# Optimization experiments

Measured on AMD Instinct MI355X. Metric: run time of the kernel, lower is better.

The kernel has to match this reference:

```python
import jax, jax.numpy as jnp
import numpy as np

B, T, D = 2, 2048, 1024
H, G, K = 16, 4, 64          # num_heads, num_kv_heads, head_dim
R = H // G                   # GQA repeat factor
F = 4096                     # mlp_dim
EPS = 1e-6


def rms_norm(x, scale, eps=EPS):
    var = jnp.mean(x.astype(jnp.float32) ** 2, axis=-1, keepdims=True)
    normed = x * jax.lax.rsqrt(var + eps)
    return (scale * normed).astype(x.dtype)


def apply_rope(x_BTHK, sin_BTK, cos_BTK):
    half = x_BTHK.shape[-1] // 2
    x1, x2 = x_BTHK[..., :half], x_BTHK[..., half:]
    s = sin_BTK[:, :, None, :]
    c = cos_BTK[:, :, None, :]
    return jnp.concatenate([x1 * c - x2 * s, x2 * c + x1 * s], axis=-1).astype(x_BTHK.dtype)


def setup_inputs() -> dict:
    key = jax.random.key(0)
    ks = jax.random.split(key, 12)
    hidden_BTD = jax.random.normal(ks[0], (B, T, D), jnp.float32)
    # rope tables: realistic sin/cos of position*inv_freq
    inv_freq = 1.0 / (10000.0 ** (jnp.arange(K // 2, dtype=jnp.float32) / (K // 2)))
    ang = jnp.arange(T, dtype=jnp.float32)[:, None] * inv_freq[None, :]  # [T, K/2]
    sin_BTK = jnp.broadcast_to(jnp.sin(ang)[None], (B, T, K // 2))
    cos_BTK = jnp.broadcast_to(jnp.cos(ang)[None], (B, T, K // 2))
    mask = jnp.broadcast_to(jnp.tril(jnp.ones((T, T), bool))[None], (B, T, T))
    sc = 1.0 / np.sqrt(D)
    scf = 1.0 / np.sqrt(F)
    return {
        "hidden_BTD": hidden_BTD, "sin_BTK": sin_BTK, "cos_BTK": cos_BTK, "mask": mask,
        "ln1_scale": jnp.ones((D,), jnp.float32),
        "ln2_scale": jnp.ones((D,), jnp.float32),
        "qn_scale": jnp.ones((K,), jnp.float32),
        "kn_scale": jnp.ones((K,), jnp.float32),
        "q_w": jax.random.normal(ks[1], (D, H * K), jnp.float32) * sc,
        "k_w": jax.random.normal(ks[2], (D, G * K), jnp.float32) * sc,
        "v_w": jax.random.normal(ks[3], (D, G * K), jnp.float32) * sc,
        "o_w": jax.random.normal(ks[4], (H * K, D), jnp.float32) * sc,
        "gate_w": jax.random.normal(ks[5], (D, F), jnp.float32) * sc,
        "up_w": jax.random.normal(ks[6], (D, F), jnp.float32) * sc,
        "down_w": jax.random.normal(ks[7], (F, D), jnp.float32) * scf,
    }


def reference(hidden_BTD, sin_BTK, cos_BTK, mask, ln1_scale, ln2_scale,
              qn_scale, kn_scale, q_w, k_w, v_w, o_w, gate_w, up_w, down_w):
    x = rms_norm(hidden_BTD, ln1_scale)
    q = rms_norm((x @ q_w).reshape(B, T, H, K), qn_scale)
    k = rms_norm((x @ k_w).reshape(B, T, G, K), kn_scale)
    v = (x @ v_w).reshape(B, T, G, K)
    q = apply_rope(q, sin_BTK, cos_BTK)
    k = apply_rope(k, sin_BTK, cos_BTK)
    q_BTGRK = q.reshape(B, T, G, R, K)
    scale = K ** (-0.5)
    logits = jnp.einsum('BTGRK,BSGK->BTSGR', q_BTGRK, k) * scale
    neg = float(jnp.finfo(logits.dtype).min)
    logits = jnp.where(mask[:, :, :, None, None], logits, neg)
    weights = jax.nn.softmax(logits.astype(jnp.float32), axis=2).astype(logits.dtype)
    attn = jnp.einsum('BTSGR,BSGK->BTGRK', weights, v).reshape(B, T, H * K)
    hidden_BTD = hidden_BTD + attn @ o_w
    y = rms_norm(hidden_BTD, ln2_scale)
    ff = (jax.nn.silu(y @ gate_w) * (y @ up_w)) @ down_w
    return hidden_BTD + ff
```

## Files before the change

### kernel.cpp

```cpp
#include <hip/hip_runtime.h>
#include <hip/hip_bf16.h>

#define EPSF 1e-6f
constexpr int Bsz  = 2;
constexpr int Tseq = 2048;
constexpr int Dmod = 1024;
constexpr int Hh   = 16;
constexpr int Gg   = 4;
constexpr int Ff   = 4096;
constexpr int Mrows = Bsz * Tseq;

typedef __attribute__((ext_vector_type(8))) short bf16x8;
typedef __attribute__((ext_vector_type(4))) float f32x4;
typedef unsigned short u16;

__device__ inline u16 f2bf(float x) {
    union { float f; unsigned u; } v; v.f = x;
    unsigned r = v.u + 0x7fff + ((v.u >> 16) & 1);
    return (u16)(r >> 16);
}
__device__ inline float bf2f(u16 h) {
    union { unsigned u; float f; } v; v.u = ((unsigned)h) << 16; return v.f;
}

__device__ __forceinline__ void async_copy16(const u16* g, u16* l) {
    __builtin_amdgcn_global_load_lds(
        (const __attribute__((address_space(1))) void*)g,
        (__attribute__((address_space(3))) void*)l, 16, 0, 0);
}


__global__ __launch_bounds__(256) void wprep_all_kernel(
    const float* __restrict__ q_w, const float* __restrict__ k_w,
    const float* __restrict__ v_w, const float* __restrict__ o_w,
    const float* __restrict__ gate_w, const float* __restrict__ up_w,
    const float* __restrict__ down_w,
    const float* __restrict__ hidden, const float* __restrict__ ln1,
    u16* __restrict__ QKVT, u16* __restrict__ OTh, u16* __restrict__ OTl,
    u16* __restrict__ GTh, u16* __restrict__ UTh, u16* __restrict__ DTh,
    u16* __restrict__ Xh)
{
    const int bx = blockIdx.x;

    if (bx >= 14848) {
        const int row = bx - 14848;
        const int tid = threadIdx.x;
        const float4 v = reinterpret_cast<const float4*>(hidden + (size_t)row * Dmod)[tid];
        float ss = v.x * v.x + v.y * v.y + v.z * v.z + v.w * v.w;
        #pragma unroll
        for (int off = 32; off; off >>= 1) ss += __shfl_xor(ss, off, 64);
        __shared__ float part[4];
        if ((tid & 63) == 0) part[tid >> 6] = ss;
        __syncthreads();
        const float tot = part[0] + part[1] + part[2] + part[3];
        const float rstd = rsqrtf(tot * (1.0f / Dmod) + EPSF);
        const float4 sc = reinterpret_cast<const float4*>(ln1)[tid];
        ushort4 h;
        h.x = f2bf(v.x * rstd * sc.x); h.y = f2bf(v.y * rstd * sc.y);
        h.z = f2bf(v.z * rstd * sc.z); h.w = f2bf(v.w * rstd * sc.w);
        *reinterpret_cast<ushort4*>(&Xh[(size_t)row * Dmod + tid * 4]) = h;
        return;
    }

    const float* W; u16* Th; u16* Tl = nullptr;
    int N, Kd, ntile, ktile, drow;
    if (bx < 1024) {
        W = q_w; N = 1024; Kd = 1024; ntile = bx & 31; ktile = bx >> 5;
        Th = QKVT; drow = ntile * 32;
    } else if (bx < 1280) {
        const int i = bx - 1024;
        W = k_w; N = 256; Kd = 1024; ntile = i & 7; ktile = i >> 3;
        Th = QKVT; drow = 1024 + ntile * 32;
    } else if (bx < 1536) {
        const int i = bx - 1280;
        W = v_w; N = 256; Kd = 1024; ntile = i & 7; ktile = i >> 3;
        Th = QKVT; drow = 1280 + ntile * 32;
    } else if (bx < 2560) {
        const int i = bx - 1536;
        W = o_w; N = 1024; Kd = 1024; ntile = i & 31; ktile = i >> 5;
        Th = OTh; Tl = OTl; drow = ntile * 32;
    } else if (bx < 6656) {
        const int i = bx - 2560;
        W = gate_w; N = 4096; Kd = 1024; ntile = i & 127; ktile = i >> 7;
        Th = GTh; drow = ntile * 32;
    } else if (bx < 10752) {
        const int i = bx - 6656;
        W = up_w; N = 4096; Kd = 1024; ntile = i & 127; ktile = i >> 7;
        Th = UTh; drow = ntile * 32;
    } else {
        const int i = bx - 10752;
        W = down_w; N = 1024; Kd = 4096; ntile = i & 31; ktile = i >> 5;
        Th = DTh; drow = ntile * 32;
    }
    const int n0 = ntile * 32, k0 = ktile * 32;

    __shared__ float tile[32][33];
    const int r = threadIdx.x >> 3, c4 = (threadIdx.x & 7) * 4;
    const float4 v = *reinterpret_cast<const float4*>(&W[(size_t)(k0 + r) * N + n0 + c4]);
    tile[r][c4 + 0] = v.x; tile[r][c4 + 1] = v.y;
    tile[r][c4 + 2] = v.z; tile[r][c4 + 3] = v.w;
    __syncthreads();
    const int nl = threadIdx.x >> 3, kq = (threadIdx.x & 7) * 4;
    float x0 = tile[kq + 0][nl], x1 = tile[kq + 1][nl];
    float x2 = tile[kq + 2][nl], x3 = tile[kq + 3][nl];
    ushort4 h;
    h.x = f2bf(x0); h.y = f2bf(x1); h.z = f2bf(x2); h.w = f2bf(x3);
    *reinterpret_cast<ushort4*>(&Th[(size_t)(drow + nl) * Kd + k0 + kq]) = h;
    if (Tl) {
        ushort4 l;
        l.x = f2bf(x0 - bf2f(h.x)); l.y = f2bf(x1 - bf2f(h.y));
        l.z = f2bf(x2 - bf2f(h.z)); l.w = f2bf(x3 - bf2f(h.w));
        *reinterpret_cast<ushort4*>(&Tl[(size_t)(drow + nl) * Kd + k0 + kq]) = l;
    }
}

template <int LO>
__global__ __launch_bounds__(256) void rmsnorm_split_kernel(
    const float* __restrict__ x, const float* __restrict__ scale,
    u16* __restrict__ oh, u16* __restrict__ ol)
{
    const int row = blockIdx.x;
    const int tid = threadIdx.x;
    const float4 v = reinterpret_cast<const float4*>(x + (size_t)row * Dmod)[tid];
    float ss = v.x * v.x + v.y * v.y + v.z * v.z + v.w * v.w;
    #pragma unroll
    for (int off = 32; off; off >>= 1) ss += __shfl_xor(ss, off, 64);
    __shared__ float part[4];
    if ((tid & 63) == 0) part[tid >> 6] = ss;
    __syncthreads();
    const float tot = part[0] + part[1] + part[2] + part[3];
    const float rstd = rsqrtf(tot * (1.0f / Dmod) + EPSF);
    const float4 sc = reinterpret_cast<const float4*>(scale)[tid];
    float o0 = v.x * rstd * sc.x, o1 = v.y * rstd * sc.y;
    float o2 = v.z * rstd * sc.z, o3 = v.w * rstd * sc.w;
    ushort4 h;
    h.x = f2bf(o0); h.y = f2bf(o1); h.z = f2bf(o2); h.w = f2bf(o3);
    *reinterpret_cast<ushort4*>(&oh[(size_t)row * Dmod + tid * 4]) = h;
    if (LO) {
        ushort4 l;
        l.x = f2bf(o0 - bf2f(h.x)); l.y = f2bf(o1 - bf2f(h.y));
        l.z = f2bf(o2 - bf2f(h.z)); l.w = f2bf(o3 - bf2f(h.w));
        *reinterpret_cast<ushort4*>(&ol[(size_t)row * Dmod + tid * 4]) = l;
    }
}

template <int NKT, int BN, int ASPLIT, int BSPLIT, int RES>
__global__ __launch_bounds__(256, 2) void mfma_gemm_pipe(
    const u16* __restrict__ Ah, const u16* __restrict__ Al,
    const u16* __restrict__ Bh, const u16* __restrict__ Bl,
    const float* __restrict__ res, float* __restrict__ C,
    int M, int N)
{
    constexpr int Kd = NKT * 32;
    constexpr int NT = (BN / 2) / 16;
    constexpr int NI = 2 + 2 * ASPLIT + (BN / 64) + (BN / 64) * BSPLIT;
    static_assert(NKT % 4 == 0 && NKT >= 8, "4-buffer rotation");

    __shared__ u16 AsH[4][128 * 32];
    __shared__ u16 BsH[4][BN * 32];
    __shared__ u16 AsL[ASPLIT ? 4 : 1][128 * 32];
    __shared__ u16 BsL[BSPLIT ? 4 : 1][BN * 32];

    const int tid = threadIdx.x;
    const int lane = tid & 63, wave = tid >> 6;
    const int wm = (wave >> 1) * 64, wn = (wave & 1) * (BN / 2);
    const int m0 = blockIdx.y * 128, n0 = blockIdx.x * BN;
    const int fm = lane & 15, quad = lane >> 4;
    const int fsw = (fm >> 1) & 3;
    const int fcol = (quad ^ fsw) * 8;

    f32x4 acc[4][NT];
    #pragma unroll
    for (int i = 0; i < 4; ++i)
        #pragma unroll
        for (int j = 0; j < NT; ++j) acc[i][j] = (f32x4){0.f, 0.f, 0.f, 0.f};

    const int srow = tid >> 2;
    const int schk = tid & 3;
    const int sw   = schk ^ ((srow >> 1) & 3);
    const u16* aS0 = &Ah[(size_t)(m0 + srow) * Kd + sw * 8];
    const u16* aS1 = &Ah[(size_t)(m0 + srow + 64) * Kd + sw * 8];
    const u16* bS0 = &Bh[(size_t)(n0 + srow) * Kd + sw * 8];
    const u16* bS1 = (BN == 128) ? &Bh[(size_t)(n0 + srow + 64) * Kd + sw * 8] : nullptr;
    const u16* alS0 = ASPLIT ? &Al[(size_t)(m0 + srow) * Kd + sw * 8] : nullptr;
    const u16* alS1 = ASPLIT ? &Al[(size_t)(m0 + srow + 64) * Kd + sw * 8] : nullptr;
    const u16* blS0 = BSPLIT ? &Bl[(size_t)(n0 + srow) * Kd + sw * 8] : nullptr;
    const u16* blS1 = (BSPLIT && BN == 128) ? &Bl[(size_t)(n0 + srow + 64) * Kd + sw * 8] : nullptr;
    const int dst0 = srow * 32 + schk * 8;
    const int dst1 = dst0 + 64 * 32;

#define PSTAGE(T, BUF) do {                                                  \
        async_copy16(aS0 + (T) * 32, &AsH[BUF][dst0]);                       \
        async_copy16(aS1 + (T) * 32, &AsH[BUF][dst1]);                       \
        if (ASPLIT) {                                                        \
            async_copy16(alS0 + (T) * 32, &AsL[BUF][dst0]);                  \
            async_copy16(alS1 + (T) * 32, &AsL[BUF][dst1]);                  \
        }                                                                    \
        async_copy16(bS0 + (T) * 32, &BsH[BUF][dst0]);                       \
        if (BN == 128) async_copy16(bS1 + (T) * 32, &BsH[BUF][dst1]);        \
        if (BSPLIT) {                                                        \
            async_copy16(blS0 + (T) * 32, &BsL[BUF][dst0]);                  \
            if (BN == 128) async_copy16(blS1 + (T) * 32, &BsL[BUF][dst1]);   \
        }                                                                    \
    } while (0)

#define PGATE(GATE) do {                                                     \
        if ((GATE) == 2) {                                                   \
            if constexpr (NI == 4)                                           \
                asm volatile("s_waitcnt vmcnt(8)" ::: "memory");             \
            else                                                             \
                asm volatile("s_waitcnt vmcnt(16)" ::: "memory");            \
        } else if ((GATE) == 1) {                                            \
            if constexpr (NI == 4)                                           \
                asm volatile("s_waitcnt vmcnt(4)" ::: "memory");             \
            else                                                             \
                asm volatile("s_waitcnt vmcnt(8)" ::: "memory");             \
        } else if ((GATE) == 0) {                                            \
            asm volatile("s_waitcnt vmcnt(0)" ::: "memory");                 \
        }                                                                    \
    } while (0)

#define PSTEP(BC, BN_, T, PF, GATE) do {                                     \
    bf16x8 ah[4], bh[NT], al[4], bl[NT];                                     \
    _Pragma("unroll")                                                        \
    for (int t = 0; t < 4; ++t) {                                            \
        const int ra = (wm + t * 16 + fm) * 32 + fcol;                       \
        ah[t] = *reinterpret_cast<const bf16x8*>(&AsH[BC][ra]);              \
        if (ASPLIT) al[t] = *reinterpret_cast<const bf16x8*>(&AsL[BC][ra]);  \
    }                                                                        \
    _Pragma("unroll")                                                        \
    for (int t = 0; t < NT; ++t) {                                           \
        const int rb = (wn + t * 16 + fm) * 32 + fcol;                       \
        bh[t] = *reinterpret_cast<const bf16x8*>(&BsH[BC][rb]);              \
        if (BSPLIT) bl[t] = *reinterpret_cast<const bf16x8*>(&BsL[BC][rb]);  \
    }                                                                        \
    if (PF) PSTAGE((T) + 3, BN_);                                            \
    __builtin_amdgcn_s_setprio(1);                                           \
    _Pragma("unroll")                                                        \
    for (int mt = 0; mt < 4; ++mt)                                           \
        _Pragma("unroll")                                                    \
        for (int nt = 0; nt < NT; ++nt) {                                    \
            acc[mt][nt] = __builtin_amdgcn_mfma_f32_16x16x32_bf16(           \
                ah[mt], bh[nt], acc[mt][nt], 0, 0, 0);                       \
            if (BSPLIT)                                                      \
                acc[mt][nt] = __builtin_amdgcn_mfma_f32_16x16x32_bf16(       \
                    ah[mt], bl[nt], acc[mt][nt], 0, 0, 0);                   \
            if (ASPLIT)                                                      \
                acc[mt][nt] = __builtin_amdgcn_mfma_f32_16x16x32_bf16(       \
                    al[mt], bh[nt], acc[mt][nt], 0, 0, 0);                   \
        }                                                                    \
    __builtin_amdgcn_s_setprio(0);                                           \
    PGATE(GATE);                                                             \
    __builtin_amdgcn_s_barrier();                                            \
} while (0)

    PSTAGE(0, 0);
    PSTAGE(1, 1);
    PSTAGE(2, 2);
    PGATE(2);
    __builtin_amdgcn_s_barrier();

    #pragma unroll 1
    for (int t4 = 0; t4 < NKT - 4; t4 += 4) {
        PSTEP((t4 + 0) & 3, (t4 + 3) & 3, t4 + 0, true, 2);
        PSTEP((t4 + 1) & 3, (t4 + 0) & 3, t4 + 1, true, 2);
        PSTEP((t4 + 2) & 3, (t4 + 1) & 3, t4 + 2, true, 2);
        PSTEP((t4 + 3) & 3, (t4 + 2) & 3, t4 + 3, true, 2);
    }
    PSTEP(0, 3, NKT - 4, true, 2);
    PSTEP(1, 0, NKT - 3, false, 1);
    PSTEP(2, 1, NKT - 2, false, 0);
    PSTEP(3, 2, NKT - 1, false, -1);

#undef PSTEP
#undef PGATE
#undef PSTAGE

    const int cr = (lane >> 4) * 4, cn = lane & 15;
    #pragma unroll
    for (int mt = 0; mt < 4; ++mt)
        #pragma unroll
        for (int nt = 0; nt < NT; ++nt)
            #pragma unroll
            for (int r = 0; r < 4; ++r) {
                const int gm = m0 + wm + mt * 16 + cr + r;
                const int gn = n0 + wn + nt * 16 + cn;
                float v = acc[mt][nt][r];
                if (RES) v += res[(size_t)gm * N + gn];
                C[(size_t)gm * N + gn] = v;
            }
}

__global__ __launch_bounds__(256, 2) void qkv_fused_kernel(
    const u16* __restrict__ Ah, const u16* __restrict__ Bh,
    const float* __restrict__ qn, const float* __restrict__ kn,
    const float* __restrict__ sinp, const float* __restrict__ cosp,
    u16* __restrict__ Qbh, u16* __restrict__ Qbl,
    u16* __restrict__ Kbh, u16* __restrict__ Kbl,
    u16* __restrict__ Vth, u16* __restrict__ Vtl)
{
    constexpr int Kd = 1024;
    constexpr int NKT = 32;
    __shared__ u16 As[4][128 * 32];
    __shared__ u16 Bs[4][128 * 32];

    const int tid = threadIdx.x;
    const int lane = tid & 63, wave = tid >> 6;
    const int wm = (wave >> 1) * 64, wn = (wave & 1) * 64;
    const int m0 = blockIdx.y * 128, n0 = blockIdx.x * 128;
    const int fm = lane & 15, quad = lane >> 4;
    const int fsw = (fm >> 1) & 3;
    const int fcol = ((quad ^ fsw) * 8);

    f32x4 acc[4][4];
    #pragma unroll
    for (int i = 0; i < 4; ++i)
        #pragma unroll
        for (int j = 0; j < 4; ++j) acc[i][j] = (f32x4){0.f, 0.f, 0.f, 0.f};

    const int srow = tid >> 2;
    const int schk = tid & 3;
    const int sw   = schk ^ ((srow >> 1) & 3);
    const u16* aS0 = &Ah[(size_t)(m0 + srow) * Kd + sw * 8];
    const u16* aS1 = &Ah[(size_t)(m0 + srow + 64) * Kd + sw * 8];
    const u16* bS0 = &Bh[(size_t)(n0 + srow) * Kd + sw * 8];
    const u16* bS1 = &Bh[(size_t)(n0 + srow + 64) * Kd + sw * 8];
    const int dst0 = srow * 32 + schk * 8;
    const int dst1 = dst0 + 64 * 32;

#define QSTAGE(T, BUF) do {                                                  \
        async_copy16(aS0 + (T) * 32, &As[BUF][dst0]);                        \
        async_copy16(aS1 + (T) * 32, &As[BUF][dst1]);                        \
        async_copy16(bS0 + (T) * 32, &Bs[BUF][dst0]);                        \
        async_copy16(bS1 + (T) * 32, &Bs[BUF][dst1]);                        \
    } while (0)

#define QSTEP(BC, BN, T, PF, GATE) do {                                      \
    bf16x8 ah[4], bh[4];                                                     \
    _Pragma("unroll")                                                        \
    for (int t = 0; t < 4; ++t) {                                            \
        ah[t] = *reinterpret_cast<const bf16x8*>(                            \
            &As[BC][(wm + t * 16 + fm) * 32 + fcol]);                        \
        bh[t] = *reinterpret_cast<const bf16x8*>(                            \
            &Bs[BC][(wn + t * 16 + fm) * 32 + fcol]);                        \
    }                                                                        \
    if (PF) QSTAGE((T) + 3, BN);                                             \
    __builtin_amdgcn_s_setprio(1);                                           \
    _Pragma("unroll")                                                        \
    for (int mt = 0; mt < 4; ++mt)                                           \
        _Pragma("unroll")                                                    \
        for (int nt = 0; nt < 4; ++nt)                                       \
            acc[mt][nt] = __builtin_amdgcn_mfma_f32_16x16x32_bf16(           \
                ah[mt], bh[nt], acc[mt][nt], 0, 0, 0);                       \
    __builtin_amdgcn_s_setprio(0);                                           \
    if ((GATE) == 2) {                                                       \
        asm volatile("s_waitcnt vmcnt(8)" ::: "memory");                     \
    } else if ((GATE) == 1) {                                                \
        asm volatile("s_waitcnt vmcnt(4)" ::: "memory");                     \
    } else if ((GATE) == 0) {                                                \
        asm volatile("s_waitcnt vmcnt(0)" ::: "memory");                     \
    }                                                                        \
    __builtin_amdgcn_s_barrier();                                            \
} while (0)

    QSTAGE(0, 0);
    QSTAGE(1, 1);
    QSTAGE(2, 2);
    asm volatile("s_waitcnt vmcnt(8)" ::: "memory");
    __builtin_amdgcn_s_barrier();

    #pragma unroll 1
    for (int t4 = 0; t4 < NKT - 4; t4 += 4) {
        QSTEP((t4 + 0) & 3, (t4 + 3) & 3, t4 + 0, true, 2);
        QSTEP((t4 + 1) & 3, (t4 + 0) & 3, t4 + 1, true, 2);
        QSTEP((t4 + 2) & 3, (t4 + 1) & 3, t4 + 2, true, 2);
        QSTEP((t4 + 3) & 3, (t4 + 2) & 3, t4 + 3, true, 2);
    }
    QSTEP(0, 3, NKT - 4, true, 2);
    QSTEP(1, 0, NKT - 3, false, 1);
    QSTEP(2, 1, NKT - 2, false, 0);
    QSTEP(3, 2, NKT - 1, false, -1);

#undef QSTEP
#undef QSTAGE

    const int gn0 = n0 + wn;
    const int l15 = lane & 15;

    if (gn0 < 1280) {
        const bool isQ = (gn0 < 1024);
        const float* nsc = isQ ? qn : kn;
        const float osc = isQ ? 0.125f : 1.0f;
        u16* __restrict__ oh = isQ ? Qbh : Kbh;
        u16* __restrict__ ol = isQ ? Qbl : Kbl;
        const int rowstride = isQ ? 1024 : 256;
        const int colbase = isQ ? gn0 : gn0 - 1024;
        float sc[4];
        #pragma unroll
        for (int nt = 0; nt < 4; ++nt) sc[nt] = nsc[nt * 16 + l15];

        #pragma unroll
        for (int mt = 0; mt < 4; ++mt)
            #pragma unroll
            for (int r = 0; r < 4; ++r) {
                const int bt = m0 + wm + mt * 16 + quad * 4 + r;
                float v[4];
                #pragma unroll
                for (int nt = 0; nt < 4; ++nt) v[nt] = acc[mt][nt][r];
                float ss = v[0] * v[0] + v[1] * v[1] + v[2] * v[2] + v[3] * v[3];
                #pragma unroll
                for (int off = 1; off < 16; off <<= 1)
                    ss += __shfl_xor(ss, off, 16);
                const float rstd = rsqrtf(ss * (1.0f / 64.0f) + EPSF);
                float nv[4];
                #pragma unroll
                for (int nt = 0; nt < 4; ++nt) nv[nt] = v[nt] * rstd * sc[nt];
                const float s0 = sinp[bt * 32 + l15];
                const float c0 = cosp[bt * 32 + l15];
                const float s1 = sinp[bt * 32 + 16 + l15];
                const float c1 = cosp[bt * 32 + 16 + l15];
                float o[4];
                o[0] = (nv[0] * c0 - nv[2] * s0) * osc;
                o[1] = (nv[1] * c1 - nv[3] * s1) * osc;
                o[2] = (nv[2] * c0 + nv[0] * s0) * osc;
                o[3] = (nv[3] * c1 + nv[1] * s1) * osc;
                #pragma unroll
                for (int nt = 0; nt < 4; ++nt) {
                    const size_t off = (size_t)bt * rowstride + colbase + nt * 16 + l15;
                    const u16 hi = f2bf(o[nt]);
                    oh[off] = hi;
                    ol[off] = f2bf(o[nt] - bf2f(hi));
                }
            }
    } else {
        const int g = (gn0 - 1280) >> 6;
        const int b = (m0 + wm) >> 11;
        const int tb = ((m0 + wm) & 2047) + quad * 4;
        #pragma unroll
        for (int mt = 0; mt < 4; ++mt)
            #pragma unroll
            for (int nt = 0; nt < 4; ++nt) {
                const float v0 = acc[mt][nt][0], v1 = acc[mt][nt][1];
                const float v2 = acc[mt][nt][2], v3 = acc[mt][nt][3];
                ushort4 hv, lv;
                hv.x = f2bf(v0); hv.y = f2bf(v1); hv.z = f2bf(v2); hv.w = f2bf(v3);
                lv.x = f2bf(v0 - bf2f(hv.x)); lv.y = f2bf(v1 - bf2f(hv.y));
                lv.z = f2bf(v2 - bf2f(hv.z)); lv.w = f2bf(v3 - bf2f(hv.w));
                const size_t off =
                    ((size_t)((b * 4 + g) * 64 + nt * 16 + l15)) * Tseq + tb + mt * 16;
                *reinterpret_cast<ushort4*>(&Vth[off]) = hv;
                *reinterpret_cast<ushort4*>(&Vtl[off]) = lv;
            }
    }
}

#define GU_MFMA4(MBASE, AF)                                                      \
    _Pragma("unroll")                                                            \
    for (int mf = 0; mf < 4; ++mf) {                                             \
        accg[(MBASE) + mf][0] = __builtin_amdgcn_mfma_f32_16x16x32_bf16(         \
            AF[mf], bgf[0], accg[(MBASE) + mf][0], 0, 0, 0);                     \
        accu[(MBASE) + mf][0] = __builtin_amdgcn_mfma_f32_16x16x32_bf16(         \
            AF[mf], buf2[0], accu[(MBASE) + mf][0], 0, 0, 0);                    \
        accg[(MBASE) + mf][1] = __builtin_amdgcn_mfma_f32_16x16x32_bf16(         \
            AF[mf], bgf[1], accg[(MBASE) + mf][1], 0, 0, 0);                     \
        accu[(MBASE) + mf][1] = __builtin_amdgcn_mfma_f32_16x16x32_bf16(         \
            AF[mf], buf2[1], accu[(MBASE) + mf][1], 0, 0, 0);                    \
    }

__global__ __launch_bounds__(512, 2) void gateup8_kernel(
    const u16* __restrict__ Yh, const u16* __restrict__ Yl,
    const u16* __restrict__ Gw, const u16* __restrict__ Uw,
    u16* __restrict__ FF)
{
    constexpr int NK = 32;
    __shared__ u16 AsH[3][256 * 32];
    __shared__ u16 AsL[3][256 * 32];
    __shared__ u16 Gs[3][128 * 32];
    __shared__ u16 Us[3][128 * 32];

    const int tid  = threadIdx.x;
    const int lane = tid & 63;
    const int wave = tid >> 6;
    const int wave_m = wave >> 2;
    const int wave_n = wave & 3;

    const int wg  = blockIdx.x;
    const int xcd = wg & 7;
    const int idx = wg >> 3;
    const int ntile = xcd * 4 + (idx & 3);
    const int mtile = idx >> 2;
    const int m0 = mtile * 256, n0 = ntile * 128;

    const int fm = lane & 15, quad = lane >> 4;
    const int fsw = (fm >> 1) & 3;
    const int fcol = (quad ^ fsw) * 8;

    f32x4 accg[8][2], accu[8][2];
    #pragma unroll
    for (int i = 0; i < 8; ++i)
        #pragma unroll
        for (int j = 0; j < 2; ++j) {
            accg[i][j] = (f32x4){0.f, 0.f, 0.f, 0.f};
            accu[i][j] = (f32x4){0.f, 0.f, 0.f, 0.f};
        }

    const int srow = tid >> 2;
    const int schk = tid & 3;
    const int sw   = schk ^ ((srow >> 1) & 3);
    const u16* aSrc0 = &Yh[(size_t)(m0 + srow) * 1024 + sw * 8];
    const u16* aSrc1 = &Yh[(size_t)(m0 + srow + 128) * 1024 + sw * 8];
    const u16* lSrc0 = &Yl[(size_t)(m0 + srow) * 1024 + sw * 8];
    const u16* lSrc1 = &Yl[(size_t)(m0 + srow + 128) * 1024 + sw * 8];
    const u16* gSrc  = &Gw[(size_t)(n0 + srow) * 1024 + sw * 8];
    const u16* uSrc  = &Uw[(size_t)(n0 + srow) * 1024 + sw * 8];
    const int aDst0 = srow * 32 + schk * 8;
    const int aDst1 = aDst0 + 128 * 32;

#define STAGE_AH(T, BUF) do {                                  \
        async_copy16(aSrc0 + (T) * 32, &AsH[BUF][aDst0]);      \
        async_copy16(aSrc1 + (T) * 32, &AsH[BUF][aDst1]); } while (0)
#define STAGE_AL(T, BUF) do {                                  \
        async_copy16(lSrc0 + (T) * 32, &AsL[BUF][aDst0]);      \
        async_copy16(lSrc1 + (T) * 32, &AsL[BUF][aDst1]); } while (0)
#define STAGE_B(T, BUF) do {                                   \
        async_copy16(gSrc + (T) * 32, &Gs[BUF][aDst0]);        \
        async_copy16(uSrc + (T) * 32, &Us[BUF][aDst0]); } while (0)

    int raOff[8], rbOff[2];
    #pragma unroll
    for (int mf = 0; mf < 8; ++mf)
        raOff[mf] = (wave_m * 128 + mf * 16 + fm) * 32 + fcol;
    #pragma unroll
    for (int nf = 0; nf < 2; ++nf)
        rbOff[nf] = (wave_n * 32 + nf * 16 + fm) * 32 + fcol;

    STAGE_AH(0, 0); STAGE_AL(0, 0); STAGE_B(0, 0);
    STAGE_AH(1, 1); STAGE_AL(1, 1); STAGE_B(1, 1);
    asm volatile("s_waitcnt vmcnt(6)" ::: "memory");
    __builtin_amdgcn_s_barrier();

#define GU_STEP(BC, BN_, T, PF, GATE) do {                                   \
    bf16x8 bgf[2], buf2[2];                                                  \
    _Pragma("unroll")                                                        \
    for (int nf = 0; nf < 2; ++nf) {                                         \
        bgf[nf]  = *reinterpret_cast<const bf16x8*>(&Gs[BC][rbOff[nf]]);     \
        buf2[nf] = *reinterpret_cast<const bf16x8*>(&Us[BC][rbOff[nf]]);     \
    }                                                                        \
    {                                                                        \
        bf16x8 af[4];                                                        \
        _Pragma("unroll")                                                    \
        for (int mf = 0; mf < 4; ++mf)                                       \
            af[mf] = *reinterpret_cast<const bf16x8*>(&AsH[BC][raOff[mf]]);  \
        if (PF) STAGE_AH((T) + 2, BN_);                                      \
        __builtin_amdgcn_s_setprio(1);                                       \
        GU_MFMA4(0, af);                                                     \
        __builtin_amdgcn_s_setprio(0);                                       \
    }                                                                        \
    {                                                                        \
        bf16x8 af[4];                                                        \
        _Pragma("unroll")                                                    \
        for (int mf = 0; mf < 4; ++mf)                                       \
            af[mf] = *reinterpret_cast<const bf16x8*>(&AsH[BC][raOff[mf + 4]]); \
        if (PF) STAGE_AL((T) + 2, BN_);                                      \
        __builtin_amdgcn_s_setprio(1);                                       \
        GU_MFMA4(4, af);                                                     \
        __builtin_amdgcn_s_setprio(0);                                       \
    }                                                                        \
    {                                                                        \
        bf16x8 af[4];                                                        \
        _Pragma("unroll")                                                    \
        for (int mf = 0; mf < 4; ++mf)                                       \
            af[mf] = *reinterpret_cast<const bf16x8*>(&AsL[BC][raOff[mf]]);  \
        if (PF) STAGE_B((T) + 2, BN_);                                       \
        __builtin_amdgcn_s_setprio(1);                                       \
        GU_MFMA4(0, af);                                                     \
        __builtin_amdgcn_s_setprio(0);                                       \
    }                                                                        \
    {                                                                        \
        bf16x8 af[4];                                                        \
        _Pragma("unroll")                                                    \
        for (int mf = 0; mf < 4; ++mf)                                       \
            af[mf] = *reinterpret_cast<const bf16x8*>(&AsL[BC][raOff[mf + 4]]); \
        __builtin_amdgcn_s_setprio(1);                                       \
        GU_MFMA4(4, af);                                                     \
        __builtin_amdgcn_s_setprio(0);                                       \
    }                                                                        \
    if ((GATE) == 1) {                                                       \
        asm volatile("s_waitcnt vmcnt(6)" ::: "memory");                     \
    } else if ((GATE) == 0) {                                                \
        asm volatile("s_waitcnt vmcnt(0)" ::: "memory");                     \
    }                                                                        \
    __builtin_amdgcn_s_barrier();                                            \
} while (0)

    #pragma unroll 1
    for (int t3 = 0; t3 < NK - 2; t3 += 3) {
        GU_STEP(0, 2, t3 + 0, true, 1);
        GU_STEP(1, 0, t3 + 1, true, 1);
        GU_STEP(2, 1, t3 + 2, true, 1);
    }
    GU_STEP(0, 2, 30, false, 0);
    GU_STEP(1, 0, 31, false, -1);

#undef GU_STEP
#undef STAGE_AH
#undef STAGE_AL
#undef STAGE_B

    const int cr = quad * 4;
    #pragma unroll
    for (int mf = 0; mf < 8; ++mf)
        #pragma unroll
        for (int nf = 0; nf < 2; ++nf)
            #pragma unroll
            for (int r = 0; r < 4; ++r) {
                const int gm = m0 + wave_m * 128 + mf * 16 + cr + r;
                const int gn = n0 + wave_n * 32 + nf * 16 + fm;
                const float g = accg[mf][nf][r];
                const float ff = (g / (1.0f + __expf(-g))) * accu[mf][nf][r];
                FF[(size_t)gm * Ff + gn] = f2bf(ff);
            }
}

__global__ __launch_bounds__(512) void attn_mfma_kernel(
    const u16* __restrict__ Qh, const u16* __restrict__ Ql,
    const u16* __restrict__ Kh, const u16* __restrict__ Kl,
    const u16* __restrict__ Vth, const u16* __restrict__ Vtl,
    u16* __restrict__ AOh, u16* __restrict__ AOl)
{
    __shared__ u16 KsH[64 * 72];
    __shared__ u16 KsL[64 * 72];
    __shared__ u16 VsH[64 * 72];
    __shared__ u16 VsL[64 * 72];
    __shared__ u16 Ps[8][16 * 72];

    const int tid = threadIdx.x;
    const int wave = tid >> 6, lane = tid & 63;
    const int l15 = lane & 15, quad = lane >> 4;

    const int bg = blockIdx.x & 7;
    const int b = bg >> 2, g = bg & 3;
    const int pair = 63 - (blockIdx.x >> 3);
    const int win = pair * 2 + (wave >> 2);
    const int t0 = win * 16;
    const int h = g * 4 + (wave & 3);

    bf16x8 qh[2], ql[2];
    {
        const size_t qrow = (size_t)(b * Tseq + t0 + l15) * 1024 + h * 64;
        #pragma unroll
        for (int ks = 0; ks < 2; ++ks) {
            qh[ks] = *reinterpret_cast<const bf16x8*>(&Qh[qrow + ks * 32 + quad * 8]);
            ql[ks] = *reinterpret_cast<const bf16x8*>(&Ql[qrow + ks * 32 + quad * 8]);
        }
    }

    const int srow = tid >> 3;
    const int scol = (tid & 7) * 8;
    const size_t kgb = (size_t)(b * Tseq) * 256 + g * 64 + scol;
    const size_t vgb = (size_t)(bg * 64 + srow) * Tseq + scol;

    const int nit = (pair * 32 + 16) / 64 + 1;

    uint4 ck0, cl0, cv0, cw0;
    {
        const size_t ka = kgb + (size_t)srow * 256;
        ck0 = *reinterpret_cast<const uint4*>(&Kh[ka]);
        cl0 = *reinterpret_cast<const uint4*>(&Kl[ka]);
        cv0 = *reinterpret_cast<const uint4*>(&Vth[vgb]);
        cw0 = *reinterpret_cast<const uint4*>(&Vtl[vgb]);
    }

    f32x4 oacc[4];
    #pragma unroll
    for (int nt = 0; nt < 4; ++nt) oacc[nt] = (f32x4){0.f, 0.f, 0.f, 0.f};
    float m_r[4], l_r[4];
    #pragma unroll
    for (int r = 0; r < 4; ++r) { m_r[r] = -1e30f; l_r[r] = 0.0f; }

    u16* psw = &Ps[wave][0];
    const int lb = srow * 72 + scol;

    for (int it = 0; it < nit; ++it) {
        const int s0 = it * 64;
        const bool diag = (it == nit - 1);

        __syncthreads();
        *reinterpret_cast<uint4*>(&KsH[lb]) = ck0;
        *reinterpret_cast<uint4*>(&KsL[lb]) = cl0;
        *reinterpret_cast<uint4*>(&VsH[lb]) = cv0;
        *reinterpret_cast<uint4*>(&VsL[lb]) = cw0;
        if (it + 1 < nit) {
            const size_t ka = kgb + (size_t)(s0 + 64 + srow) * 256;
            ck0 = *reinterpret_cast<const uint4*>(&Kh[ka]);
            cl0 = *reinterpret_cast<const uint4*>(&Kl[ka]);
            const size_t va = vgb + s0 + 64;
            cv0 = *reinterpret_cast<const uint4*>(&Vth[va]);
            cw0 = *reinterpret_cast<const uint4*>(&Vtl[va]);
        }
        __syncthreads();

        f32x4 sacc[4];
        #pragma unroll
        for (int nt = 0; nt < 4; ++nt) sacc[nt] = (f32x4){0.f, 0.f, 0.f, 0.f};

        #pragma unroll
        for (int ks = 0; ks < 2; ++ks) {
            bf16x8 kfh[4], kfl[4];
            #pragma unroll
            for (int nt = 0; nt < 4; ++nt) {
                const int a = (nt * 16 + l15) * 72 + ks * 32 + quad * 8;
                kfh[nt] = *reinterpret_cast<const bf16x8*>(&KsH[a]);
                kfl[nt] = *reinterpret_cast<const bf16x8*>(&KsL[a]);
            }
            #pragma unroll
            for (int nt = 0; nt < 4; ++nt) {
                sacc[nt] = __builtin_amdgcn_mfma_f32_16x16x32_bf16(qh[ks], kfh[nt], sacc[nt], 0, 0, 0);
                sacc[nt] = __builtin_amdgcn_mfma_f32_16x16x32_bf16(ql[ks], kfh[nt], sacc[nt], 0, 0, 0);
                sacc[nt] = __builtin_amdgcn_mfma_f32_16x16x32_bf16(qh[ks], kfl[nt], sacc[nt], 0, 0, 0);
            }
        }

        if (diag) {
            #pragma unroll
            for (int nt = 0; nt < 4; ++nt) {
                const int sg = s0 + nt * 16 + l15;
                #pragma unroll
                for (int r = 0; r < 4; ++r)
                    if (sg > t0 + quad * 4 + r) sacc[nt][r] = -1e30f;
            }
        }

        #pragma unroll
        for (int r = 0; r < 4; ++r) {
            float mx = fmaxf(fmaxf(sacc[0][r], sacc[1][r]),
                             fmaxf(sacc[2][r], sacc[3][r]));
            #pragma unroll
            for (int off = 1; off < 16; off <<= 1)
                mx = fmaxf(mx, __shfl_xor(mx, off, 16));
            const float mnew = fmaxf(m_r[r], mx);
            const float alpha = __expf(m_r[r] - mnew);
            m_r[r] = mnew;

            float rs = 0.0f;
            #pragma unroll
            for (int nt = 0; nt < 4; ++nt) {
                const float p = __expf(sacc[nt][r] - mnew);
                sacc[nt][r] = p;
                rs += p;
            }
            #pragma unroll
            for (int off = 1; off < 16; off <<= 1)
                rs += __shfl_xor(rs, off, 16);
            l_r[r] = l_r[r] * alpha + rs;
            #pragma unroll
            for (int nt = 0; nt < 4; ++nt) oacc[nt][r] *= alpha;
            #pragma unroll
            for (int nt = 0; nt < 4; ++nt)
                psw[(quad * 4 + r) * 72 + nt * 16 + l15] = f2bf(sacc[nt][r]);
        }

        #pragma unroll
        for (int ks = 0; ks < 2; ++ks) {
            const bf16x8 pa = *reinterpret_cast<const bf16x8*>(
                &psw[l15 * 72 + ks * 32 + quad * 8]);
            bf16x8 vfh[4], vfl[4];
            #pragma unroll
            for (int nt = 0; nt < 4; ++nt) {
                const int a = (nt * 16 + l15) * 72 + ks * 32 + quad * 8;
                vfh[nt] = *reinterpret_cast<const bf16x8*>(&VsH[a]);
                vfl[nt] = *reinterpret_cast<const bf16x8*>(&VsL[a]);
            }
            #pragma unroll
            for (int nt = 0; nt < 4; ++nt) {
                oacc[nt] = __builtin_amdgcn_mfma_f32_16x16x32_bf16(pa, vfh[nt], oacc[nt], 0, 0, 0);
                oacc[nt] = __builtin_amdgcn_mfma_f32_16x16x32_bf16(pa, vfl[nt], oacc[nt], 0, 0, 0);
            }
        }
    }

    #pragma unroll
    for (int r = 0; r < 4; ++r) {
        const float inv = 1.0f / l_r[r];
        const size_t orow = (size_t)(b * Tseq + t0 + quad * 4 + r) * 1024 + h * 64;
        #pragma unroll
        for (int nt = 0; nt < 4; ++nt) {
            const float o = oacc[nt][r] * inv;
            const u16 hi = f2bf(o);
            AOh[orow + nt * 16 + l15] = hi;
            AOl[orow + nt * 16 + l15] = f2bf(o - bf2f(hi));
        }
    }
}

extern "C" void kernel_launch(void* const* d_in, const int* in_sizes, int n_in,
                              void* d_out, int out_size, void* d_ws,
                              size_t ws_size, hipStream_t stream)
{
    const float* hidden = (const float*)d_in[0];
    const float* sinp   = (const float*)d_in[1];
    const float* cosp   = (const float*)d_in[2];
    const float* ln1    = (const float*)d_in[4];
    const float* ln2    = (const float*)d_in[5];
    const float* qn     = (const float*)d_in[6];
    const float* kn     = (const float*)d_in[7];
    const float* q_w    = (const float*)d_in[8];
    const float* k_w    = (const float*)d_in[9];
    const float* v_w    = (const float*)d_in[10];
    const float* o_w    = (const float*)d_in[11];
    const float* gate_w = (const float*)d_in[12];
    const float* up_w   = (const float*)d_in[13];
    const float* down_w = (const float*)d_in[14];
    float* out = (float*)d_out;

    char* base = (char*)d_ws;
    u16*   OTh  = (u16*)(base);
    u16*   OTl  = (u16*)(base + 2097152);
    u16*   GTh  = (u16*)(base + 4194304);
    u16*   UTh  = (u16*)(base + 12582912);
    u16*   DTh  = (u16*)(base + 20971520);
    u16*   QKVT = (u16*)(base + 29360128);
    u16*   Xh   = (u16*)(base + 32505856);
    u16*   Qbh  = (u16*)(base + 40894464);
    u16*   Qbl  = (u16*)(base + 49283072);
    u16*   Kbh  = (u16*)(base + 57671680);
    u16*   Kbl  = (u16*)(base + 59768832);
    u16*   Vth  = (u16*)(base + 61865984);
    u16*   Vtl  = (u16*)(base + 63963136);
    u16*   AOh  = (u16*)(base + 66060288);
    u16*   AOl  = (u16*)(base + 74448896);
    u16*   FFh  = (u16*)(base + 82837504);

    float* H2 = (float*)Qbh;
    u16*   Yh = Kbh;
    u16*   Yl = AOh;

    wprep_all_kernel<<<14848 + Mrows, 256, 0, stream>>>(
        q_w, k_w, v_w, o_w, gate_w, up_w, down_w, hidden, ln1,
        QKVT, OTh, OTl, GTh, UTh, DTh, Xh);

    qkv_fused_kernel<<<dim3(12, 32), 256, 0, stream>>>(
        Xh, QKVT, qn, kn, sinp, cosp, Qbh, Qbl, Kbh, Kbl, Vth, Vtl);

    attn_mfma_kernel<<<Bsz * Gg * (Tseq / 32), 512, 0, stream>>>(
        Qbh, Qbl, Kbh, Kbl, Vth, Vtl, AOh, AOl);

    mfma_gemm_pipe<32, 128, 1, 1, 1><<<dim3(8, 32), 256, 0, stream>>>(
        AOh, AOl, OTh, OTl, hidden, H2, Mrows, Dmod);

    rmsnorm_split_kernel<1><<<Mrows, 256, 0, stream>>>(H2, ln2, Yh, Yl);

    gateup8_kernel<<<512, 512, 0, stream>>>(Yh, Yl, GTh, UTh, FFh);

    mfma_gemm_pipe<128, 128, 0, 0, 1><<<dim3(8, 32), 256, 0, stream>>>(
        FFh, nullptr, DTh, nullptr, H2, out, Mrows, Dmod);
}
```

Baseline: 490.0 us.

## Reshape gate/up GEMM wave tiling from 2x4 to 4x2 with square 64x64 wave tiles

Changes the per-wave sub-tile in the fused gate/up GEMM from 128 rows by 32 columns to 64 by 64, arranging the 8 waves as 4x2 instead of 2x4. Each wave now loads 4 A fragments per hi/lo half and 4 B fragments each for gate and up, instead of 8 A and 2 B. This cuts LDS read traffic per MFMA, since the square tile gives better operand reuse. It also restructures the prefetch interleave into two blocks with two MFMA groups each, and raises live B-fragment registers.

```diff
diff --git a/kernel.cpp b/kernel.cpp
--- a/kernel.cpp
+++ b/kernel.cpp
@@ -454,17 +454,17 @@
     }
 }
 
-#define GU_MFMA4(MBASE, AF)                                                      \
+#define GU_MFMA8(AF, NB0)                                                        \
     _Pragma("unroll")                                                            \
     for (int mf = 0; mf < 4; ++mf) {                                             \
-        accg[(MBASE) + mf][0] = __builtin_amdgcn_mfma_f32_16x16x32_bf16(         \
-            AF[mf], bgf[0], accg[(MBASE) + mf][0], 0, 0, 0);                     \
-        accu[(MBASE) + mf][0] = __builtin_amdgcn_mfma_f32_16x16x32_bf16(         \
-            AF[mf], buf2[0], accu[(MBASE) + mf][0], 0, 0, 0);                    \
-        accg[(MBASE) + mf][1] = __builtin_amdgcn_mfma_f32_16x16x32_bf16(         \
-            AF[mf], bgf[1], accg[(MBASE) + mf][1], 0, 0, 0);                     \
-        accu[(MBASE) + mf][1] = __builtin_amdgcn_mfma_f32_16x16x32_bf16(         \
-            AF[mf], buf2[1], accu[(MBASE) + mf][1], 0, 0, 0);                    \
+        accg[mf][(NB0)] = __builtin_amdgcn_mfma_f32_16x16x32_bf16(               \
+            AF[mf], bgf[(NB0)], accg[mf][(NB0)], 0, 0, 0);                       \
+        accu[mf][(NB0)] = __builtin_amdgcn_mfma_f32_16x16x32_bf16(               \
+            AF[mf], buf2[(NB0)], accu[mf][(NB0)], 0, 0, 0);                      \
+        accg[mf][(NB0) + 1] = __builtin_amdgcn_mfma_f32_16x16x32_bf16(           \
+            AF[mf], bgf[(NB0) + 1], accg[mf][(NB0) + 1], 0, 0, 0);               \
+        accu[mf][(NB0) + 1] = __builtin_amdgcn_mfma_f32_16x16x32_bf16(           \
+            AF[mf], buf2[(NB0) + 1], accu[mf][(NB0) + 1], 0, 0, 0);              \
     }
 
 __global__ __launch_bounds__(512, 2) void gateup8_kernel(
@@ -481,8 +481,8 @@
     const int tid  = threadIdx.x;
     const int lane = tid & 63;
     const int wave = tid >> 6;
-    const int wave_m = wave >> 2;
-    const int wave_n = wave & 3;
+    const int wave_m = wave >> 1;
+    const int wave_n = wave & 1;
 
     const int wg  = blockIdx.x;
     const int xcd = wg & 7;
@@ -495,11 +495,11 @@
     const int fsw = (fm >> 1) & 3;
     const int fcol = (quad ^ fsw) * 8;
 
-    f32x4 accg[8][2], accu[8][2];
-    #pragma unroll
-    for (int i = 0; i < 8; ++i)
-        #pragma unroll
-        for (int j = 0; j < 2; ++j) {
+    f32x4 accg[4][4], accu[4][4];
+    #pragma unroll
+    for (int i = 0; i < 4; ++i)
+        #pragma unroll
+        for (int j = 0; j < 4; ++j) {
             accg[i][j] = (f32x4){0.f, 0.f, 0.f, 0.f};
             accu[i][j] = (f32x4){0.f, 0.f, 0.f, 0.f};
         }
@@ -526,13 +526,13 @@
         async_copy16(gSrc + (T) * 32, &Gs[BUF][aDst0]);        \
         async_copy16(uSrc + (T) * 32, &Us[BUF][aDst0]); } while (0)
 
-    int raOff[8], rbOff[2];
-    #pragma unroll
-    for (int mf = 0; mf < 8; ++mf)
-        raOff[mf] = (wave_m * 128 + mf * 16 + fm) * 32 + fcol;
-    #pragma unroll
-    for (int nf = 0; nf < 2; ++nf)
-        rbOff[nf] = (wave_n * 32 + nf * 16 + fm) * 32 + fcol;
+    int raOff[4], rbOff[4];
+    #pragma unroll
+    for (int mf = 0; mf < 4; ++mf)
+        raOff[mf] = (wave_m * 64 + mf * 16 + fm) * 32 + fcol;
+    #pragma unroll
+    for (int nf = 0; nf < 4; ++nf)
+        rbOff[nf] = (wave_n * 64 + nf * 16 + fm) * 32 + fcol;
 
     STAGE_AH(0, 0); STAGE_AL(0, 0); STAGE_B(0, 0);
     STAGE_AH(1, 1); STAGE_AL(1, 1); STAGE_B(1, 1);
@@ -540,49 +540,37 @@
     __builtin_amdgcn_s_barrier();
 
 #define GU_STEP(BC, BN_, T, PF, GATE) do {                                   \
-    bf16x8 bgf[2], buf2[2];                                                  \
+    bf16x8 bgf[4], buf2[4];                                                  \
     _Pragma("unroll")                                                        \
-    for (int nf = 0; nf < 2; ++nf) {                                         \
+    for (int nf = 0; nf < 4; ++nf) {                                         \
         bgf[nf]  = *reinterpret_cast<const bf16x8*>(&Gs[BC][rbOff[nf]]);     \
         buf2[nf] = *reinterpret_cast<const bf16x8*>(&Us[BC][rbOff[nf]]);     \
     }                                                                        \
     {                                                                        \
-        bf16x8 af[4];                                                        \
+        bf16x8 ahf[4];                                                       \
         _Pragma("unroll")                                                    \
         for (int mf = 0; mf < 4; ++mf)                                       \
-            af[mf] = *reinterpret_cast<const bf16x8*>(&AsH[BC][raOff[mf]]);  \
+            ahf[mf] = *reinterpret_cast<const bf16x8*>(&AsH[BC][raOff[mf]]); \
         if (PF) STAGE_AH((T) + 2, BN_);                                      \
         __builtin_amdgcn_s_setprio(1);                                       \
-        GU_MFMA4(0, af);                                                     \
+        GU_MFMA8(ahf, 0);                                                    \
+        __builtin_amdgcn_s_setprio(0);                                       \
+        if (PF) STAGE_AL((T) + 2, BN_);                                      \
+        __builtin_amdgcn_s_setprio(1);                                       \
+        GU_MFMA8(ahf, 2);                                                    \
         __builtin_amdgcn_s_setprio(0);                                       \
     }                                                                        \
     {                                                                        \
-        bf16x8 af[4];                                                        \
+        bf16x8 alf[4];                                                       \
         _Pragma("unroll")                                                    \
         for (int mf = 0; mf < 4; ++mf)                                       \
-            af[mf] = *reinterpret_cast<const bf16x8*>(&AsH[BC][raOff[mf + 4]]); \
-        if (PF) STAGE_AL((T) + 2, BN_);                                      \
-        __builtin_amdgcn_s_setprio(1);                                       \
-        GU_MFMA4(4, af);                                                     \
-        __builtin_amdgcn_s_setprio(0);                                       \
-    }                                                                        \
-    {                                                                        \
-        bf16x8 af[4];                                                        \
-        _Pragma("unroll")                                                    \
-        for (int mf = 0; mf < 4; ++mf)                                       \
-            af[mf] = *reinterpret_cast<const bf16x8*>(&AsL[BC][raOff[mf]]);  \
+            alf[mf] = *reinterpret_cast<const bf16x8*>(&AsL[BC][raOff[mf]]); \
         if (PF) STAGE_B((T) + 2, BN_);                                       \
         __builtin_amdgcn_s_setprio(1);                                       \
-        GU_MFMA4(0, af);                                                     \
+        GU_MFMA8(alf, 0);                                                    \
         __builtin_amdgcn_s_setprio(0);                                       \
-    }                                                                        \
-    {                                                                        \
-        bf16x8 af[4];                                                        \
-        _Pragma("unroll")                                                    \
-        for (int mf = 0; mf < 4; ++mf)                                       \
-            af[mf] = *reinterpret_cast<const bf16x8*>(&AsL[BC][raOff[mf + 4]]); \
         __builtin_amdgcn_s_setprio(1);                                       \
-        GU_MFMA4(4, af);                                                     \
+        GU_MFMA8(alf, 2);                                                    \
         __builtin_amdgcn_s_setprio(0);                                       \
     }                                                                        \
     if ((GATE) == 1) {                                                       \
@@ -609,13 +597,13 @@
 
     const int cr = quad * 4;
     #pragma unroll
-    for (int mf = 0; mf < 8; ++mf)
-        #pragma unroll
-        for (int nf = 0; nf < 2; ++nf)
+    for (int mf = 0; mf < 4; ++mf)
+        #pragma unroll
+        for (int nf = 0; nf < 4; ++nf)
             #pragma unroll
             for (int r = 0; r < 4; ++r) {
-                const int gm = m0 + wave_m * 128 + mf * 16 + cr + r;
-                const int gn = n0 + wave_n * 32 + nf * 16 + fm;
+                const int gm = m0 + wave_m * 64 + mf * 16 + cr + r;
+                const int gn = n0 + wave_n * 64 + nf * 16 + fm;
                 const float g = accg[mf][nf][r];
                 const float ff = (g / (1.0f + __expf(-g))) * accu[mf][nf][r];
                 FF[(size_t)gm * Ff + gn] = f2bf(ff);
```

Result: no change. 485.9 us (-0.8%).
